# Performance work log

Measured on AMD Instinct MI355X. Metric: run time of the kernel, lower is better.

Reference implementation:

```python
import jax, jax.numpy as jnp
import numpy as np

S = 512          # number of scenes (sequences)
P = 128          # pedestrians per scene
G = 16           # groups per scene (labels 1..G, each of size P//G)
D_IN, D_HID, D_OUT, D_FINAL = 256, 512, 16, 64


def setup_inputs() -> dict:
    key = jax.random.key(0)
    ks = jax.random.split(key, 10)
    B = S * P
    h_states = jax.random.normal(ks[0], (B, D_IN), dtype=jnp.float32)
    end_pos = jax.random.normal(ks[1], (B, 2), dtype=jnp.float32)
    starts = jnp.arange(S, dtype=jnp.int64) * P
    seq_start_end = jnp.stack([starts, starts + P], axis=1)
    # labels 1..G within each scene; every group present -> n_group = G (static)
    end_group = ((jnp.arange(B, dtype=jnp.int64) % G) + 1).reshape(B, 1)
    s = 0.05  # scale randn params to keep activations tame
    W_intra_0 = s * jax.random.normal(ks[2], (D_IN, D_HID), dtype=jnp.float32)
    W_intra_1 = s * jax.random.normal(ks[3], (D_HID, D_OUT), dtype=jnp.float32)
    W_inter_0 = s * jax.random.normal(ks[4], (D_OUT, D_HID), dtype=jnp.float32)
    W_inter_1 = s * jax.random.normal(ks[5], (D_HID, D_OUT), dtype=jnp.float32)
    out_W = s * jax.random.normal(ks[6], (2 * D_OUT, D_FINAL), dtype=jnp.float32)
    out_b = jnp.zeros((D_FINAL,), dtype=jnp.float32)
    return {"h_states": h_states, "end_pos": end_pos,
            "seq_start_end": seq_start_end, "end_group": end_group,
            "W_intra_0": W_intra_0, "W_intra_1": W_intra_1,
            "W_inter_0": W_inter_0, "W_inter_1": W_inter_1,
            "out_W": out_W, "out_b": out_b}


def reference(h_states, end_pos, seq_start_end, end_group,
              W_intra_0, W_intra_1, W_inter_0, W_inter_1, out_W, out_b):
    B = h_states.shape[0]
    num_seq = seq_start_end.shape[0]
    P_ = B // num_seq
    labels = end_group.reshape(num_seq, P_)
    h_seq = h_states.reshape(num_seq, P_, -1)
    eye = jnp.eye(P_, dtype=bool)
    grp_ids = jnp.arange(1, G + 1)

    def per_scene(h, lab):
        # intra-group adjacency: same nonzero group, plus self loops
        M = ((lab[:, None] == lab[None, :]) & (lab[:, None] != 0)) | eye
        Mf = M.astype(h.dtype)
        A = Mf / jnp.sum(Mf, axis=1, keepdims=True)          # row-normalize
        H = jax.nn.relu((A @ h) @ W_intra_0)
        H_intra = jax.nn.relu((A @ H) @ W_intra_1)           # (P, D_OUT)
        # GPool: unique rows of M == one-hot group membership (all labels nonzero)
        onehot = (lab[None, :] == grp_ids[:, None]).astype(h.dtype)  # (G, P)
        R = onehot / jnp.sum(onehot, axis=1, keepdims=True)
        Hg = R @ H_intra                                     # (G, D_OUT)
        # inter-group GCN over fully-connected normalized adjacency
        Ai = jnp.full((G, G), 1.0 / G, dtype=h.dtype)
        Hg = jax.nn.relu((Ai @ Hg) @ W_inter_0)
        Hg = jax.nn.relu((Ai @ Hg) @ W_inter_1)
        H_inter = R.T @ Hg                                   # GUnpool: (P, D_OUT)
        cat = jnp.concatenate([H_intra, H_inter], axis=1)    # (P, 2*D_OUT)
        return cat @ out_W + out_b

    out = jax.vmap(per_scene)(h_seq, labels)
    return out.reshape(B, -1)
```

## Files before the change

kernel.cpp:

```cpp
#include <hip/hip_runtime.h>
#include <hip/hip_bf16.h>

#define S_SCENES 512
#define P_PED    128
#define G_GRP    16
#define D_IN     256
#define D_HID    512
#define D_OUT    16
#define D_FINAL  64

typedef __bf16 bf16x8 __attribute__((ext_vector_type(8)));
typedef float  f32x4  __attribute__((ext_vector_type(4)));

#define HGS 264
#define Y1S 520

__device__ __forceinline__ unsigned short f2bf(float f) {
  unsigned int x; __builtin_memcpy(&x, &f, 4);
  unsigned int r = x + 0x7FFFu + ((x >> 16) & 1u);
  return (unsigned short)(r >> 16);
}

__global__ void build_wfrag(const float* __restrict__ W0,
                            const float* __restrict__ W1,
                            unsigned short* __restrict__ W0F,
                            unsigned short* __restrict__ W1F) {
  int tid = blockIdx.x * blockDim.x + threadIdx.x;
  if (tid < 131072) {
    int k = tid >> 9, n = tid & 511;
    float v = W0[tid];
    int k8 = k >> 5, kr = k & 31;
    int j = kr & 7, lhi = kr >> 3;
    int nt = n >> 4, n16 = n & 15;
    int l = lhi * 16 + n16;
    W0F[(((k8 * 32 + nt) * 64) + l) * 8 + j] = f2bf(v);
  } else {
    int t2 = tid - 131072;
    if (t2 < 8192) {
      int k = t2 >> 4, n = t2 & 15;
      float v = W1[t2];
      int ks = k >> 5, kr = k & 31;
      int j = kr & 7, lhi = kr >> 3;
      int l = lhi * 16 + n;
      W1F[((ks * 64) + l) * 8 + j] = f2bf(v);
    }
  }
}

__global__ __launch_bounds__(512, 2) void scene_kernel(
    const float* __restrict__ h,
    const int* __restrict__ sse,
    const int* __restrict__ grp,
    const unsigned short* __restrict__ W0F,
    const unsigned short* __restrict__ W1F,
    const float* __restrict__ Wi0,
    const float* __restrict__ Wi1,
    const float* __restrict__ Wout,
    const float* __restrict__ bout,
    float* __restrict__ out)
{
  __shared__ int lab[P_PED];
  __shared__ int cnt[G_GRP];
  __shared__ unsigned char members[G_GRP][P_PED];
  __shared__ unsigned short hg[G_GRP * HGS];
  __shared__ unsigned short y1[G_GRP * Y1S];
  __shared__ float hg2p[8][G_GRP][D_OUT];
  __shared__ float hg2[G_GRP][D_OUT];
  __shared__ float mvec[D_OUT];
  __shared__ float t1v[D_HID];
  __shared__ float hiv[D_OUT];
  __shared__ float cvec[D_FINAL];
  __shared__ float orow[G_GRP * D_FINAL];

  const int t = threadIdx.x;
  const int s = blockIdx.x;
  const int is64 = (grp[1] == 0) ? 1 : 0;
  const int start = is64 ? sse[4 * s] : sse[2 * s];
  const int w = t >> 6;
  const int l = t & 63;
  const int m16 = l & 15;
  const int q = l >> 4;

  if (t < G_GRP) cnt[t] = 0;
  __syncthreads();
  if (t < P_PED) {
    int idx = start + t;
    int g = (is64 ? grp[2 * idx] : grp[idx]) - 1;
    if (g < 0) g = 0; if (g > G_GRP - 1) g = G_GRP - 1;
    lab[t] = g;
    int slot = atomicAdd(&cnt[g], 1);
    if (slot < P_PED) members[g][slot] = (unsigned char)t;
  }
  __syncthreads();

  {
    int g0 = w;
    int g1 = w + 8;
    int ch = (t & 63) << 2;
    int cn0 = cnt[g0], cn1 = cnt[g1];
    const float* base = h + (size_t)start * D_IN + ch;
    f32x4 a0 = {0.f, 0.f, 0.f, 0.f}, a1 = {0.f, 0.f, 0.f, 0.f};
    if (cn0 == 8 && cn1 == 8) {
      #pragma unroll
      for (int m = 0; m < 8; ++m) {
        int p0 = members[g0][m];
        int p1 = members[g1][m];
        a0 += *(const f32x4*)(base + p0 * D_IN);
        a1 += *(const f32x4*)(base + p1 * D_IN);
      }
      a0 *= 0.125f; a1 *= 0.125f;
    } else {
      for (int m = 0; m < cn0; ++m) a0 += *(const f32x4*)(base + members[g0][m] * D_IN);
      for (int m = 0; m < cn1; ++m) a1 += *(const f32x4*)(base + members[g1][m] * D_IN);
      a0 *= 1.0f / (float)(cn0 > 0 ? cn0 : 1);
      a1 *= 1.0f / (float)(cn1 > 0 ? cn1 : 1);
    }
    ushort4 o0, o1;
    o0.x = f2bf(a0[0]); o0.y = f2bf(a0[1]); o0.z = f2bf(a0[2]); o0.w = f2bf(a0[3]);
    o1.x = f2bf(a1[0]); o1.y = f2bf(a1[1]); o1.z = f2bf(a1[2]); o1.w = f2bf(a1[3]);
    *(ushort4*)&hg[g0 * HGS + ch] = o0;
    *(ushort4*)&hg[g1 * HGS + ch] = o1;
  }
  __syncthreads();

  bf16x8 afr[8];
  #pragma unroll
  for (int k8 = 0; k8 < 8; ++k8)
    afr[k8] = *(const bf16x8*)&hg[m16 * HGS + k8 * 32 + q * 8];

  #pragma unroll
  for (int ntl = 0; ntl < 4; ++ntl) {
    int nt = w * 4 + ntl;
    f32x4 acc = {0.f, 0.f, 0.f, 0.f};
    #pragma unroll
    for (int k8 = 0; k8 < 8; ++k8) {
      bf16x8 bfr = *(const bf16x8*)(W0F + (size_t)(((k8 * 32 + nt) * 64) + l) * 8);
      acc = __builtin_amdgcn_mfma_f32_16x16x32_bf16(afr[k8], bfr, acc, 0, 0, 0);
    }
    #pragma unroll
    for (int r = 0; r < 4; ++r) {
      float v = acc[r];
      v = v > 0.f ? v : 0.f;
      y1[(q * 4 + r) * Y1S + nt * 16 + m16] = f2bf(v);
    }
  }
  __syncthreads();

  {
    f32x4 acc = {0.f, 0.f, 0.f, 0.f};
    #pragma unroll
    for (int kk = 0; kk < 2; ++kk) {
      int ks = w * 2 + kk;
      bf16x8 a2 = *(const bf16x8*)&y1[m16 * Y1S + ks * 32 + q * 8];
      bf16x8 b2 = *(const bf16x8*)(W1F + (size_t)(ks * 64 + l) * 8);
      acc = __builtin_amdgcn_mfma_f32_16x16x32_bf16(a2, b2, acc, 0, 0, 0);
    }
    #pragma unroll
    for (int r = 0; r < 4; ++r) hg2p[w][q * 4 + r][m16] = acc[r];
  }
  __syncthreads();
  if (t < 256) {
    int g = t >> 4, n = t & 15;
    float sum = 0.f;
    #pragma unroll
    for (int ww = 0; ww < 8; ++ww) sum += hg2p[ww][g][n];
    hg2[g][n] = sum > 0.f ? sum : 0.f;
  }
  __syncthreads();

  if (t < D_OUT) {
    float sm = 0.f;
    #pragma unroll
    for (int g = 0; g < G_GRP; ++g) sm += hg2[g][t];
    mvec[t] = sm * (1.0f / 16.0f);
  }
  __syncthreads();
  {
    float sm = 0.f;
    #pragma unroll
    for (int n = 0; n < D_OUT; ++n) sm += mvec[n] * Wi0[n * D_HID + t];
    t1v[t] = sm > 0.f ? sm : 0.f;
  }
  __syncthreads();
  #pragma unroll
  for (int nn = 0; nn < 2; ++nn) {
    int n = w * 2 + nn;
    float part = 0.f;
    #pragma unroll
    for (int r = 0; r < 8; ++r) {
      int j = l + r * 64;
      part += t1v[j] * Wi1[j * D_OUT + n];
    }
    for (int off = 32; off; off >>= 1) part += __shfl_down(part, off);
    if (l == 0) hiv[n] = part > 0.f ? part : 0.f;
  }
  __syncthreads();
  if (t < D_FINAL) {
    float sm = 0.f;
    #pragma unroll
    for (int n = 0; n < D_OUT; ++n)
      sm += hiv[n] * Wout[(G_GRP + n) * D_FINAL + t];
    cvec[t] = sm;
  }
  __syncthreads();

  for (int it = 0; it < 2; ++it) {
    int item = t + it * 512;
    int g = item >> 6, c = item & 63;
    float sm = 0.f;
    #pragma unroll
    for (int n = 0; n < D_OUT; ++n)
      sm += hg2[g][n] * Wout[n * D_FINAL + c];
    int cn = cnt[g];
    float inv = 1.0f / (float)(cn > 0 ? cn : 1);
    sm += cvec[c] * inv + bout[c];
    orow[g * D_FINAL + c] = sm;
  }
  __syncthreads();

  for (int it = 0; it < 4; ++it) {
    int i4 = t + it * 512;
    int p  = i4 >> 4;
    int c4 = i4 & 15;
    int g  = lab[p];
    float4 v = *(const float4*)&orow[g * D_FINAL + c4 * 4];
    *(float4*)(out + (size_t)(start + p) * D_FINAL + c4 * 4) = v;
  }
}

extern "C" void kernel_launch(void* const* d_in, const int* in_sizes, int n_in,
                              void* d_out, int out_size, void* d_ws, size_t ws_size,
                              hipStream_t stream) {
  const float* h    = (const float*)d_in[0];
  const int*   sse  = (const int*)d_in[2];
  const int*   grp  = (const int*)d_in[3];
  const float* W0   = (const float*)d_in[4];
  const float* W1   = (const float*)d_in[5];
  const float* Wi0  = (const float*)d_in[6];
  const float* Wi1  = (const float*)d_in[7];
  const float* Wout = (const float*)d_in[8];
  const float* bout = (const float*)d_in[9];

  unsigned short* W0F = (unsigned short*)d_ws;
  unsigned short* W1F = (unsigned short*)d_ws + 131072;

  build_wfrag<<<544, 256, 0, stream>>>(W0, W1, W0F, W1F);
  scene_kernel<<<S_SCENES, 512, 0, stream>>>(h, sse, grp, W0F, W1F,
                                             Wi0, Wi1, Wout, bout,
                                             (float*)d_out);
}
```

Measured before the change: 130.2 us.

## Stage scene hidden states into LDS as bf16 with coalesced loads, alias shared buffers

Each block now loads all 128x256 hidden-state rows of its scene into a 64KB shared buffer as bf16 using fully coalesced per-row loads. The load is issued before the group-label atomics, and the per-group mean then gathers from LDS rather than doing scattered global float4 loads. The intermediate buffers y1, hg2p, t1v and orow are aliased onto that same buffer, and launch_bounds is raised to 4 blocks per CU. The bf16 rounding before averaging changes numerics slightly, and the 64KB+ of LDS per block likely limits occupancy regardless of the launch bound.

Result: no change. 129.0 us (-0.9%).

```diff
diff --git a/kernel.cpp b/kernel.cpp
--- a/kernel.cpp
+++ b/kernel.cpp
@@ -15,6 +15,10 @@
 #define HGS 264
 #define Y1S 520
 
+__device__ __forceinline__ float bf2f(unsigned short u) {
+  unsigned int x = ((unsigned int)u) << 16;
+  float f; __builtin_memcpy(&f, &x, 4); return f;
+}
 __device__ __forceinline__ unsigned short f2bf(float f) {
   unsigned int x; __builtin_memcpy(&x, &f, 4);
   unsigned int r = x + 0x7FFFu + ((x >> 16) & 1u);
@@ -47,7 +51,7 @@
   }
 }
 
-__global__ __launch_bounds__(512, 2) void scene_kernel(
+__global__ __launch_bounds__(512, 4) void scene_kernel(
     const float* __restrict__ h,
     const int* __restrict__ sse,
     const int* __restrict__ grp,
@@ -59,18 +63,21 @@
     const float* __restrict__ bout,
     float* __restrict__ out)
 {
+  __shared__ __align__(16) unsigned char smem[65536];
   __shared__ int lab[P_PED];
   __shared__ int cnt[G_GRP];
   __shared__ unsigned char members[G_GRP][P_PED];
   __shared__ unsigned short hg[G_GRP * HGS];
-  __shared__ unsigned short y1[G_GRP * Y1S];
-  __shared__ float hg2p[8][G_GRP][D_OUT];
   __shared__ float hg2[G_GRP][D_OUT];
   __shared__ float mvec[D_OUT];
-  __shared__ float t1v[D_HID];
   __shared__ float hiv[D_OUT];
   __shared__ float cvec[D_FINAL];
-  __shared__ float orow[G_GRP * D_FINAL];
+
+  unsigned short* hlds = (unsigned short*)smem;
+  unsigned short* y1   = (unsigned short*)smem;
+  float* hg2p = (float*)(smem + 16640);
+  float* t1v  = (float*)(smem + 32768);
+  float* orow = (float*)smem;
 
   const int t = threadIdx.x;
   const int s = blockIdx.x;
@@ -83,43 +90,75 @@
 
   if (t < G_GRP) cnt[t] = 0;
   __syncthreads();
+
+  int myg = -1;
   if (t < P_PED) {
     int idx = start + t;
-    int g = (is64 ? grp[2 * idx] : grp[idx]) - 1;
+    myg = (is64 ? grp[2 * idx] : grp[idx]) - 1;
+  }
+  const float* hbase = h + (size_t)start * D_IN + (l << 2);
+  f32x4 vbuf[8];
+  #pragma unroll
+  for (int it = 0; it < 8; ++it)
+    vbuf[it] = *(const f32x4*)(hbase + (w + it * 8) * D_IN);
+
+  if (t < P_PED) {
+    int g = myg;
     if (g < 0) g = 0; if (g > G_GRP - 1) g = G_GRP - 1;
     lab[t] = g;
     int slot = atomicAdd(&cnt[g], 1);
     if (slot < P_PED) members[g][slot] = (unsigned char)t;
   }
+
+  #pragma unroll
+  for (int it = 0; it < 8; ++it) {
+    ushort4 o;
+    o.x = f2bf(vbuf[it][0]); o.y = f2bf(vbuf[it][1]);
+    o.z = f2bf(vbuf[it][2]); o.w = f2bf(vbuf[it][3]);
+    *(ushort4*)&hlds[(w + it * 8) * D_IN + (l << 2)] = o;
+  }
+  #pragma unroll
+  for (int it = 0; it < 8; ++it)
+    vbuf[it] = *(const f32x4*)(hbase + (w + 64 + it * 8) * D_IN);
+  #pragma unroll
+  for (int it = 0; it < 8; ++it) {
+    ushort4 o;
+    o.x = f2bf(vbuf[it][0]); o.y = f2bf(vbuf[it][1]);
+    o.z = f2bf(vbuf[it][2]); o.w = f2bf(vbuf[it][3]);
+    *(ushort4*)&hlds[(w + 64 + it * 8) * D_IN + (l << 2)] = o;
+  }
   __syncthreads();
 
   {
-    int g0 = w;
-    int g1 = w + 8;
-    int ch = (t & 63) << 2;
+    int g0 = w, g1 = w + 8;
     int cn0 = cnt[g0], cn1 = cnt[g1];
-    const float* base = h + (size_t)start * D_IN + ch;
     f32x4 a0 = {0.f, 0.f, 0.f, 0.f}, a1 = {0.f, 0.f, 0.f, 0.f};
     if (cn0 == 8 && cn1 == 8) {
       #pragma unroll
       for (int m = 0; m < 8; ++m) {
-        int p0 = members[g0][m];
-        int p1 = members[g1][m];
-        a0 += *(const f32x4*)(base + p0 * D_IN);
-        a1 += *(const f32x4*)(base + p1 * D_IN);
+        ushort4 u0 = *(const ushort4*)&hlds[members[g0][m] * D_IN + (l << 2)];
+        ushort4 u1 = *(const ushort4*)&hlds[members[g1][m] * D_IN + (l << 2)];
+        a0[0] += bf2f(u0.x); a0[1] += bf2f(u0.y); a0[2] += bf2f(u0.z); a0[3] += bf2f(u0.w);
+        a1[0] += bf2f(u1.x); a1[1] += bf2f(u1.y); a1[2] += bf2f(u1.z); a1[3] += bf2f(u1.w);
       }
       a0 *= 0.125f; a1 *= 0.125f;
     } else {
-      for (int m = 0; m < cn0; ++m) a0 += *(const f32x4*)(base + members[g0][m] * D_IN);
-      for (int m = 0; m < cn1; ++m) a1 += *(const f32x4*)(base + members[g1][m] * D_IN);
+      for (int m = 0; m < cn0; ++m) {
+        ushort4 u = *(const ushort4*)&hlds[members[g0][m] * D_IN + (l << 2)];
+        a0[0] += bf2f(u.x); a0[1] += bf2f(u.y); a0[2] += bf2f(u.z); a0[3] += bf2f(u.w);
+      }
+      for (int m = 0; m < cn1; ++m) {
+        ushort4 u = *(const ushort4*)&hlds[members[g1][m] * D_IN + (l << 2)];
+        a1[0] += bf2f(u.x); a1[1] += bf2f(u.y); a1[2] += bf2f(u.z); a1[3] += bf2f(u.w);
+      }
       a0 *= 1.0f / (float)(cn0 > 0 ? cn0 : 1);
       a1 *= 1.0f / (float)(cn1 > 0 ? cn1 : 1);
     }
     ushort4 o0, o1;
     o0.x = f2bf(a0[0]); o0.y = f2bf(a0[1]); o0.z = f2bf(a0[2]); o0.w = f2bf(a0[3]);
     o1.x = f2bf(a1[0]); o1.y = f2bf(a1[1]); o1.z = f2bf(a1[2]); o1.w = f2bf(a1[3]);
-    *(ushort4*)&hg[g0 * HGS + ch] = o0;
-    *(ushort4*)&hg[g1 * HGS + ch] = o1;
+    *(ushort4*)&hg[g0 * HGS + (l << 2)] = o0;
+    *(ushort4*)&hg[g1 * HGS + (l << 2)] = o1;
   }
   __syncthreads();
 
@@ -156,14 +195,15 @@
       acc = __builtin_amdgcn_mfma_f32_16x16x32_bf16(a2, b2, acc, 0, 0, 0);
     }
     #pragma unroll
-    for (int r = 0; r < 4; ++r) hg2p[w][q * 4 + r][m16] = acc[r];
+    for (int r = 0; r < 4; ++r)
+      hg2p[(w * 16 + (q * 4 + r)) * 16 + m16] = acc[r];
   }
   __syncthreads();
   if (t < 256) {
     int g = t >> 4, n = t & 15;
     float sum = 0.f;
     #pragma unroll
-    for (int ww = 0; ww < 8; ++ww) sum += hg2p[ww][g][n];
+    for (int ww = 0; ww < 8; ++ww) sum += hg2p[(ww * 16 + g) * 16 + n];
     hg2[g][n] = sum > 0.f ? sum : 0.f;
   }
   __syncthreads();
```
